# Kernel optimization log

Measured on AMD Instinct MI355X. Metric: run time of the kernel, lower is better.

Reference implementation:

```python
import jax, jax.numpy as jnp
import numpy as np

S_LEN = 256   # seq_len
B = 512       # batch
STATE = 32    # state_dim
ZD = 64       # z_dim
RNN = 512     # rnn_dim
HD = 512      # h_dim
LOG2PI = float(np.log(2.0 * np.pi))


def setup_inputs() -> dict:
    key = jax.random.key(0)
    ks = jax.random.split(key, 12)

    def mat(k, shape, fan_in):
        return jax.random.normal(k, shape, dtype=jnp.float32) * (1.0 / np.sqrt(fan_in))

    z32 = lambda *s: jnp.zeros(s, jnp.float32)
    return {
        "states": jax.random.normal(ks[0], (S_LEN, B, STATE), jnp.float32),
        "z": jax.random.normal(ks[1], (B, ZD), jnp.float32),
        # GRU layer 0: input = concat(state, action) -> 2*STATE
        "Wih0": mat(ks[2], (3 * RNN, 2 * STATE), 2 * STATE),
        "Whh0": mat(ks[3], (3 * RNN, RNN), RNN),
        "bih0": z32(3 * RNN),
        "bhh0": z32(3 * RNN),
        # GRU layer 1: input = hidden of layer 0
        "Wih1": mat(ks[4], (3 * RNN, RNN), RNN),
        "Whh1": mat(ks[5], (3 * RNN, RNN), RNN),
        "bih1": z32(3 * RNN),
        "bhh1": z32(3 * RNN),
        # dec_action_fc: Linear(STATE+ZD+RNN -> HD), ReLU, Linear(HD -> HD), ReLU
        "Wfc1": mat(ks[6], (HD, STATE + ZD + RNN), STATE + ZD + RNN),
        "bfc1": z32(HD),
        "Wfc2": mat(ks[7], (HD, HD), HD),
        "bfc2": z32(HD),
        "Wmean": mat(ks[8], (STATE, HD), HD),
        "bmean": z32(STATE),
        "Wlv": mat(ks[9], (STATE, HD), HD),
        "blv": z32(STATE),
    }


def _gru_step(x, h, Wih, Whh, bih, bhh):
    # PyTorch GRUCell math
    gi = x @ Wih.T + bih  # [B, 3R]
    gh = h @ Whh.T + bhh
    ir, iz, inn = jnp.split(gi, 3, axis=1)
    hr, hz, hn = jnp.split(gh, 3, axis=1)
    r = jax.nn.sigmoid(ir + hr)
    zg = jax.nn.sigmoid(iz + hz)
    n = jnp.tanh(inn + r * hn)
    return (1.0 - zg) * n + zg * h


def reference(states, z, Wih0, Whh0, bih0, bhh0, Wih1, Whh1, bih1, bhh1,
              Wfc1, bfc1, Wfc2, bfc2, Wmean, bmean, Wlv, blv):
    # actions[t] = states[t+1] - states[t]
    actions = states[1:] - states[:-1]
    # loop runs for actions.size(0)-1 = T-2 steps using (states[t], actions[t])
    xs = (states[:-2], actions[:-1])
    Bb = z.shape[0]
    R = Whh0.shape[1]
    h_init = jnp.zeros((2, Bb, R), states.dtype)
    nll_init = jnp.zeros((Bb, states.shape[-1]), states.dtype)

    def step(carry, xt):
        h, nll = carry
        s, a = xt  # [B, STATE] each
        # decode_action: cat(state, z, hidden[-1]) -> MLP -> mean, logvar
        fc_in = jnp.concatenate([s, z, h[1]], axis=1)
        dh = jax.nn.relu(fc_in @ Wfc1.T + bfc1)
        dh = jax.nn.relu(dh @ Wfc2.T + bfc2)
        mean = dh @ Wmean.T + bmean
        logvar = dh @ Wlv.T + blv
        # nll -= Normal(mean, logvar).log_prob(action), std = exp(0.5*logvar)
        nll_t = 0.5 * ((a - mean) ** 2 * jnp.exp(-logvar) + logvar + LOG2PI)
        # update_hidden_state with cat(state, action) through 2-layer GRU
        x_in = jnp.concatenate([s, a], axis=1)
        h0n = _gru_step(x_in, h[0], Wih0, Whh0, bih0, bhh0)
        h1n = _gru_step(h0n, h[1], Wih1, Whh1, bih1, bhh1)
        return (jnp.stack([h0n, h1n]), nll + nll_t), None

    (h, nll), _ = jax.lax.scan(step, (h_init, nll_init), xs)
    return nll  # accumulated NLL, shape [B, STATE]
```

## Files before the change

kernel.cpp:

```cpp
#include <hip/hip_runtime.h>
#include <math.h>

#define BATCH 512
#define LOG2PI 1.8378770664093453f

typedef __attribute__((ext_vector_type(8))) short bfrag;
typedef __attribute__((ext_vector_type(4))) float f32x4;
typedef __attribute__((ext_vector_type(4))) unsigned int u32x4;

#define MFMA(a,b,c) __builtin_amdgcn_mfma_f32_16x16x32_bf16(a,b,c,0,0,0)
#define ASTORE(p,v) __hip_atomic_store((p),(v),__ATOMIC_RELAXED,__HIP_MEMORY_SCOPE_AGENT)
#define ALOAD(p)    __hip_atomic_load((p),__ATOMIC_RELAXED,__HIP_MEMORY_SCOPE_AGENT)

__device__ __forceinline__ void st16_sc1(void* p, u32x4 v){
  asm volatile("global_store_dwordx4 %0, %1, off sc1" :: "v"(p), "v"(v) : "memory");
}

__device__ __forceinline__ float sigm(float x){ return 1.0f/(1.0f+__expf(-x)); }
__device__ __forceinline__ unsigned short f2bf(float f){
  unsigned int u = __builtin_bit_cast(unsigned int, f);
  u += 0x7FFFu + ((u>>16)&1u);
  return (unsigned short)(u>>16);
}
__device__ __forceinline__ bfrag cvt8(const float* __restrict__ p){
  bfrag v;
  #pragma unroll
  for (int e=0;e<8;++e) v[e] = (short)f2bf(p[e]);
  return v;
}
__device__ __forceinline__ bfrag cvt8d(const float* __restrict__ p1, const float* __restrict__ p0){
  bfrag v;
  #pragma unroll
  for (int e=0;e<8;++e) v[e] = (short)f2bf(p1[e]-p0[e]);
  return v;
}

__device__ __forceinline__ void gsync(unsigned* flags, unsigned* phase, unsigned tgt) {
  __syncthreads();
  const int tid = threadIdx.x;
  if (blockIdx.x == 0) {
    if (tid < 64) {
      if (tid == 0) ASTORE(&flags[0], tgt);
      unsigned spin = 0;
      while (true) {
        bool ok = true;
        #pragma unroll
        for (int g = 0; g < 4; ++g)
          ok &= (ALOAD(&flags[(g*64 + tid)*16]) >= tgt);
        if (__all(ok)) break;
        if (++spin > (1u<<26)) break;
        __builtin_amdgcn_s_sleep(1);
      }
      if (tid == 0) ASTORE(phase, tgt);
    }
  } else if (tid == 0) {
    ASTORE(&flags[blockIdx.x*16], tgt);
    unsigned spin = 0;
    while (ALOAD(phase) < tgt) {
      if (++spin > (1u<<26)) break;
      __builtin_amdgcn_s_sleep(1);
    }
  }
  __syncthreads();
  if (tid < 64) __builtin_amdgcn_fence(__ATOMIC_ACQUIRE, "agent");
  __syncthreads();
}

struct Params {
  const float *states, *zin;
  const float *Wih0, *Whh0, *bih0, *bhh0;
  const float *Wih1, *Whh1, *bih1, *bhh1;
  const float *Wfc1, *bfc1, *Wfc2, *bfc2;
  const float *Wmean, *bmean, *Wlv, *blv;
  unsigned short *h0b0, *h0b1, *h1b0, *h1b1;
  unsigned short *dh1b0, *dh1b1, *dh2b0, *dh2b1;
  float *out;
};

__global__ __launch_bounds__(256, 1) void fused(Params P, unsigned* flags, unsigned* phase) {
  __shared__ unsigned short sm[74752];
  const int tid  = threadIdx.x;
  const int lane = tid & 63;
  const int wv   = tid >> 6;
  const int r16  = lane & 15, kg = lane >> 4;
  const int blk  = blockIdx.x;
  const int xg   = blk & 7, sub = blk >> 3;

  unsigned short* h0b[2]  = {P.h0b0, P.h0b1};
  unsigned short* h1b[2]  = {P.h1b0, P.h1b1};
  unsigned short* dh1b[2] = {P.dh1b0, P.dh1b1};
  unsigned short* dh2b[2] = {P.dh2b0, P.dh2b1};

  if (xg < 4) {
    const int jt = sub;
    const float* Wsrc[2] = {P.Wih1, P.Whh1};
    #pragma unroll
    for (int m = 0; m < 2; ++m) {
      const float* W = Wsrc[m];
      for (int c = tid; c < 3072; c += 256) {
        int g = c >> 10, rem = c & 1023;
        int r = rem >> 6, k = (rem & 63) << 3;
        *(bfrag*)&sm[(g*16+r)*1032 + m*512 + k] =
          cvt8(&W[((size_t)(g*512 + jt*16 + r))*512 + k]);
      }
    }
  } else if (xg < 6) {
    const int jt = sub;
    for (int c = tid; c < 384; c += 256) {
      int g = c >> 7, rem = c & 127;
      int r = rem >> 3, k = (rem & 7) << 3;
      *(bfrag*)&sm[(g*16+r)*584 + k] =
        cvt8(&P.Wih0[((size_t)(g*512 + jt*16 + r))*64 + k]);
    }
    for (int c = tid; c < 3072; c += 256) {
      int g = c >> 10, rem = c & 1023;
      int r = rem >> 6, k = (rem & 63) << 3;
      *(bfrag*)&sm[(g*16+r)*584 + 64 + k] =
        cvt8(&P.Whh0[((size_t)(g*512 + jt*16 + r))*512 + k]);
    }
  } else if (xg == 6) {
    const int bn = (sub & 7) * 64;
    const int bmB = (sub >> 3) * 128;
    for (int c = tid; c < 4864; c += 256) {
      int n = c / 76, k = (c % 76) << 3;
      *(bfrag*)&sm[n*616 + k] = cvt8(&P.Wfc1[(size_t)(bn + n)*608 + k]);
    }
    for (int c = tid; c < 1024; c += 256) {
      int r = c >> 3, k = (c & 7) << 3;
      *(bfrag*)&sm[47616 + r*64 + k] = cvt8(&P.zin[(size_t)(bmB + r)*64 + k]);
    }
  } else {
    const int bn = (sub & 7) * 64;
    for (int c = tid; c < 4096; c += 256) {
      int n = c >> 6, k = (c & 63) << 3;
      *(bfrag*)&sm[n*520 + k] = cvt8(&P.Wfc2[(size_t)(bn + n)*512 + k]);
    }
    for (int c = tid; c < 4096; c += 256) {
      int m = c >> 6, k = (c & 63) << 3;
      const float* src = (m < 32) ? &P.Wmean[(size_t)m*512 + k]
                                  : &P.Wlv[(size_t)(m-32)*512 + k];
      *(bfrag*)&sm[33280 + m*520 + k] = cvt8(src);
    }
  }

  float b0 = 0.f, b1 = 0.f, b2 = 0.f, b3 = 0.f;
  if (xg < 4) {
    int j = sub*16 + r16;
    b0 = P.bih1[j] + P.bhh1[j];
    b1 = P.bih1[j+512] + P.bhh1[j+512];
    b2 = P.bih1[j+1024]; b3 = P.bhh1[j+1024];
  } else if (xg < 6) {
    int j = sub*16 + r16;
    b0 = P.bih0[j] + P.bhh0[j];
    b1 = P.bih0[j+512] + P.bhh0[j+512];
    b2 = P.bih0[j+1024]; b3 = P.bhh0[j+1024];
  } else if (xg == 6) {
    int nn0 = (sub & 7)*64 + (wv&1)*32 + r16;
    b0 = P.bfc1[nn0]; b1 = P.bfc1[nn0+16];
  } else {
    int nn0 = (sub & 7)*64 + (wv&1)*32 + r16;
    b0 = P.bfc2[nn0]; b1 = P.bfc2[nn0+16];
    int c = wv*16 + r16;
    b2 = (c < 32) ? P.bmean[c] : P.blv[c-32];
  }
  float hs[4][4] = {};
  float nacc0 = 0.f, nacc1 = 0.f;

  for (int u = 0; u <= 256; ++u) {
    gsync(flags, phase, (unsigned)(u+1));
    if (xg < 4) {
      if (u >= 1 && u <= 254) {
        const int jt = sub, bmB = xg * 128;
        const unsigned short* h0r = h0b[(u-1)&1];
        const unsigned short* h1r = h1b[u&1];
        f32x4 R[2]={}, Z[2]={}, NI[2]={}, NH[2]={};
        const int row0 = bmB + wv*32 + r16;
        #pragma unroll
        for (int half = 0; half < 2; ++half) {
          const unsigned short* asrc = half ? h1r : h0r;
          #pragma unroll 4
          for (int kt = 0; kt < 16; ++kt) {
            const int kk = kt*32 + kg*8;
            const int kl = half*512 + kk;
            bfrag a0 = *(const bfrag*)&asrc[(size_t)row0*512 + kk];
            bfrag a1 = *(const bfrag*)&asrc[(size_t)(row0+16)*512 + kk];
            bfrag bR = *(const bfrag*)&sm[(0*16+r16)*1032 + kl];
            bfrag bZ = *(const bfrag*)&sm[(1*16+r16)*1032 + kl];
            bfrag bN = *(const bfrag*)&sm[(2*16+r16)*1032 + kl];
            R[0]=MFMA(a0,bR,R[0]); R[1]=MFMA(a1,bR,R[1]);
            Z[0]=MFMA(a0,bZ,Z[0]); Z[1]=MFMA(a1,bZ,Z[1]);
            if (!half) { NI[0]=MFMA(a0,bN,NI[0]); NI[1]=MFMA(a1,bN,NI[1]); }
            else       { NH[0]=MFMA(a0,bN,NH[0]); NH[1]=MFMA(a1,bN,NH[1]); }
          }
        }
        unsigned short* exch = sm + 49536;
        #pragma unroll
        for (int fm = 0; fm < 2; ++fm)
          #pragma unroll
          for (int e = 0; e < 4; ++e) {
            int rl = wv*32 + fm*16 + kg*4 + e;
            float r  = sigm(R[fm][e] + b0);
            float zg = sigm(Z[fm][e] + b1);
            float nn = tanhf(NI[fm][e] + b2 + r*(NH[fm][e] + b3));
            float hn = (1.f - zg)*nn + zg*hs[fm][e];
            hs[fm][e] = hn;
            exch[rl*16 + r16] = f2bf(hn);
          }
        __syncthreads();
        {
          unsigned short* dst = h1b[(u-1)&1];
          int r = tid >> 1, hc = tid & 1;
          u32x4 v = *(const u32x4*)&exch[r*16 + hc*8];
          st16_sc1(dst + ((size_t)(bmB + r))*512 + jt*16 + hc*8, v);
        }
      }
    } else if (xg < 6) {
      if (u <= 253) {
        const int jt = sub, bmB = (xg - 4) * 256;
        const unsigned short* h0r = h0b[(u-1)&1];
        const float* s0 = P.states + (size_t)u*BATCH*32;
        f32x4 R[4]={}, Z[4]={}, NI[4]={}, NH[4]={};
        #pragma unroll
        for (int ks = 0; ks < 2; ++ks) {
          const int kl = ks*32 + kg*8;
          bfrag a[4];
          #pragma unroll
          for (int fm = 0; fm < 4; ++fm) {
            int row = bmB + wv*64 + fm*16 + r16;
            a[fm] = (ks == 0)
              ? cvt8(&s0[(size_t)row*32 + kg*8])
              : cvt8d(&s0[(size_t)(BATCH + row)*32 + kg*8], &s0[(size_t)row*32 + kg*8]);
          }
          bfrag bR = *(const bfrag*)&sm[(0*16+r16)*584 + kl];
          bfrag bZ = *(const bfrag*)&sm[(1*16+r16)*584 + kl];
          bfrag bN = *(const bfrag*)&sm[(2*16+r16)*584 + kl];
          #pragma unroll
          for (int fm = 0; fm < 4; ++fm) {
            R[fm]=MFMA(a[fm],bR,R[fm]); Z[fm]=MFMA(a[fm],bZ,Z[fm]); NI[fm]=MFMA(a[fm],bN,NI[fm]);
          }
        }
        #pragma unroll 2
        for (int kt = 0; kt < 16; ++kt) {
          const int kk = kt*32 + kg*8;
          const int kl = 64 + kk;
          bfrag a[4];
          #pragma unroll
          for (int fm = 0; fm < 4; ++fm) {
            int row = bmB + wv*64 + fm*16 + r16;
            a[fm] = *(const bfrag*)&h0r[(size_t)row*512 + kk];
          }
          bfrag bR = *(const bfrag*)&sm[(0*16+r16)*584 + kl];
          bfrag bZ = *(const bfrag*)&sm[(1*16+r16)*584 + kl];
          bfrag bN = *(const bfrag*)&sm[(2*16+r16)*584 + kl];
          #pragma unroll
          for (int fm = 0; fm < 4; ++fm) {
            R[fm]=MFMA(a[fm],bR,R[fm]); Z[fm]=MFMA(a[fm],bZ,Z[fm]); NH[fm]=MFMA(a[fm],bN,NH[fm]);
          }
        }
        unsigned short* exch = sm + 28032;
        #pragma unroll
        for (int fm = 0; fm < 4; ++fm)
          #pragma unroll
          for (int e = 0; e < 4; ++e) {
            int rl = wv*64 + fm*16 + kg*4 + e;
            float r  = sigm(R[fm][e] + b0);
            float zg = sigm(Z[fm][e] + b1);
            float nn = tanhf(NI[fm][e] + b2 + r*(NH[fm][e] + b3));
            float hn = (1.f - zg)*nn + zg*hs[fm][e];
            hs[fm][e] = hn;
            exch[rl*16 + r16] = f2bf(hn);
          }
        __syncthreads();
        {
          unsigned short* dst = h0b[u&1];
          int r = tid;
          u32x4 v0 = *(const u32x4*)&exch[r*16];
          u32x4 v1 = *(const u32x4*)&exch[r*16 + 8];
          unsigned short* dp = dst + ((size_t)(bmB + r))*512 + jt*16;
          st16_sc1(dp,     v0);
          st16_sc1(dp + 8, v1);
        }
      }
    } else if (xg == 6) {
      if (u >= 1 && u <= 254) {
        const int bmB = (sub >> 3) * 128, bnB = (sub & 7) * 64;
        const unsigned short* h1r = h1b[u&1];
        const float* s0 = P.states + (size_t)(u-1)*BATCH*32;
        f32x4 acc[4][2] = {};
        const int arow = bmB + (wv>>1)*64;
        const int bcol = (wv&1)*32;
        #pragma unroll 2
        for (int kt = 0; kt < 19; ++kt) {
          const int k = kt*32 + kg*8;
          bfrag a[4];
          #pragma unroll
          for (int fm = 0; fm < 4; ++fm) {
            int row = arow + fm*16 + r16;
            int rl  = row - bmB;
            if (kt == 0)      a[fm] = cvt8(&s0[(size_t)row*32 + k]);
            else if (kt <= 2) a[fm] = *(const bfrag*)&sm[47616 + rl*64 + (k - 32)];
            else              a[fm] = *(const bfrag*)&h1r[(size_t)row*512 + (k - 96)];
          }
          bfrag bf0 = *(const bfrag*)&sm[(bcol      + r16)*616 + k];
          bfrag bf1 = *(const bfrag*)&sm[(bcol + 16 + r16)*616 + k];
          #pragma unroll
          for (int fm = 0; fm < 4; ++fm) {
            acc[fm][0] = MFMA(a[fm], bf0, acc[fm][0]);
            acc[fm][1] = MFMA(a[fm], bf1, acc[fm][1]);
          }
        }
        unsigned short* exch = sm + 39424;
        #pragma unroll
        for (int fm = 0; fm < 4; ++fm)
          #pragma unroll
          for (int fn = 0; fn < 2; ++fn) {
            float bias = fn ? b1 : b0;
            #pragma unroll
            for (int e = 0; e < 4; ++e) {
              int rl = (wv>>1)*64 + fm*16 + kg*4 + e;
              int cl = bcol + fn*16 + r16;
              exch[rl*64 + cl] = f2bf(fmaxf(acc[fm][fn][e] + bias, 0.f));
            }
          }
        __syncthreads();
        {
          unsigned short* dst = dh1b[(u-1)&1];
          int r = tid >> 1, hc = tid & 1;
          #pragma unroll
          for (int q = 0; q < 4; ++q) {
            u32x4 v = *(const u32x4*)&exch[r*64 + hc*32 + q*8];
            st16_sc1(dst + ((size_t)(bmB + r))*512 + bnB + hc*32 + q*8, v);
          }
        }
        __syncthreads();
      }
    } else {
      if (u >= 2 && u <= 255) {
        const int bmB = (sub >> 3) * 128, bnB = (sub & 7) * 64;
        const unsigned short* dr = dh1b[u&1];
        f32x4 acc[4][2] = {};
        const int arow = bmB + (wv>>1)*64;
        const int bcol = (wv&1)*32;
        #pragma unroll 2
        for (int kt = 0; kt < 16; ++kt) {
          const int k = kt*32 + kg*8;
          bfrag a[4];
          #pragma unroll
          for (int fm = 0; fm < 4; ++fm) {
            int row = arow + fm*16 + r16;
            a[fm] = *(const bfrag*)&dr[(size_t)row*512 + k];
          }
          bfrag bf0 = *(const bfrag*)&sm[(bcol      + r16)*520 + k];
          bfrag bf1 = *(const bfrag*)&sm[(bcol + 16 + r16)*520 + k];
          #pragma unroll
          for (int fm = 0; fm < 4; ++fm) {
            acc[fm][0] = MFMA(a[fm], bf0, acc[fm][0]);
            acc[fm][1] = MFMA(a[fm], bf1, acc[fm][1]);
          }
        }
        unsigned short* exch = sm + 66560;
        #pragma unroll
        for (int fm = 0; fm < 4; ++fm)
          #pragma unroll
          for (int fn = 0; fn < 2; ++fn) {
            float bias = fn ? b1 : b0;
            #pragma unroll
            for (int e = 0; e < 4; ++e) {
              int rl = (wv>>1)*64 + fm*16 + kg*4 + e;
              int cl = bcol + fn*16 + r16;
              exch[rl*64 + cl] = f2bf(fmaxf(acc[fm][fn][e] + bias, 0.f));
            }
          }
        __syncthreads();
        {
          unsigned short* dst = dh2b[u&1];
          int r = tid >> 1, hc = tid & 1;
          #pragma unroll
          for (int q = 0; q < 4; ++q) {
            u32x4 v = *(const u32x4*)&exch[r*64 + hc*32 + q*8];
            st16_sc1(dst + ((size_t)(bmB + r))*512 + bnB + hc*32 + q*8, v);
          }
        }
      }
      if (u >= 3) {
        const int t = u - 3;
        const unsigned short* dr = dh2b[(u-1)&1];
        f32x4 acc = {};
        #pragma unroll 2
        for (int kt = 0; kt < 16; ++kt) {
          const int k = kt*32 + kg*8;
          bfrag a = *(const bfrag*)&dr[(size_t)(sub*16 + r16)*512 + k];
          bfrag b = *(const bfrag*)&sm[33280 + (wv*16 + r16)*520 + k];
          acc = MFMA(a, b, acc);
        }
        __syncthreads();
        float* exch = (float*)(sm + 66560);
        const int c = wv*16 + r16;
        #pragma unroll
        for (int e = 0; e < 4; ++e)
          exch[(kg*4+e)*66 + c] = acc[e] + b2;
        __syncthreads();
        const float* s0 = P.states + (size_t)t*BATCH*32;
        #pragma unroll
        for (int e2 = 0; e2 < 2; ++e2) {
          int idx = tid*2 + e2;
          int r = idx >> 5, i = idx & 31;
          int b = sub*16 + r;
          float mean = exch[r*66 + i], lv = exch[r*66 + 32 + i];
          float av = s0[(size_t)(BATCH + b)*32 + i] - s0[(size_t)b*32 + i];
          float d = av - mean;
          float v = 0.5f*(d*d*__expf(-lv) + lv + LOG2PI);
          if (e2) nacc1 += v; else nacc0 += v;
        }
      }
    }
  }

  if (xg == 7) {
    #pragma unroll
    for (int e2 = 0; e2 < 2; ++e2) {
      int idx = tid*2 + e2;
      int b = sub*16 + (idx >> 5), i = idx & 31;
      P.out[(size_t)b*32 + i] = e2 ? nacc1 : nacc0;
    }
  }
}

extern "C" void kernel_launch(void* const* d_in, const int* in_sizes, int n_in,
                              void* d_out, int out_size, void* d_ws, size_t ws_size,
                              hipStream_t stream) {
  Params P;
  P.states = (const float*)d_in[0];
  P.zin    = (const float*)d_in[1];
  P.Wih0   = (const float*)d_in[2];
  P.Whh0   = (const float*)d_in[3];
  P.bih0   = (const float*)d_in[4];
  P.bhh0   = (const float*)d_in[5];
  P.Wih1   = (const float*)d_in[6];
  P.Whh1   = (const float*)d_in[7];
  P.bih1   = (const float*)d_in[8];
  P.bhh1   = (const float*)d_in[9];
  P.Wfc1   = (const float*)d_in[10];
  P.bfc1   = (const float*)d_in[11];
  P.Wfc2   = (const float*)d_in[12];
  P.bfc2   = (const float*)d_in[13];
  P.Wmean  = (const float*)d_in[14];
  P.bmean  = (const float*)d_in[15];
  P.Wlv    = (const float*)d_in[16];
  P.blv    = (const float*)d_in[17];
  P.out = (float*)d_out;

  const size_t HB = (size_t)512*512;
  unsigned short* u = (unsigned short*)d_ws;
  P.h0b0 = u;        P.h0b1 = u + HB;
  P.h1b0 = u + 2*HB; P.h1b1 = u + 3*HB;
  P.dh1b0 = u + 4*HB; P.dh1b1 = u + 5*HB;
  P.dh2b0 = u + 6*HB; P.dh2b1 = u + 7*HB;
  unsigned* flags = (unsigned*)(u + 8*HB);
  unsigned* phase = flags + 256*16;

  hipMemsetAsync(u, 0, 4*HB*sizeof(unsigned short), stream);
  hipMemsetAsync(flags, 0, (256*16 + 16)*sizeof(unsigned), stream);
  hipMemsetAsync(d_out, 0, (size_t)out_size*sizeof(float), stream);

  fused<<<dim3(256), dim3(256), 0, stream>>>(P, flags, phase);
}
```

Baseline: 4.660 ms.

## Replace global barrier with per-producer dataflow flags and triple-buffered activations

Removes the centralized grid barrier, where block 0 polled every block and then released them all. Each block now waits only on the specific producer blocks whose outputs it reads, checking their flags at step u or u-1, and publishes its own flag after finishing the step. Activation buffers go from double to triple buffering so that blocks up to one step apart do not overwrite data still being read. This cuts the barrier's round-trip latency and lets stages drift relative to each other, at the cost of more workspace and intricate dependency indexing that must be exactly right for correctness.

```diff
diff --git a/kernel.cpp b/kernel.cpp
--- a/kernel.cpp
+++ b/kernel.cpp
@@ -33,37 +33,6 @@
   #pragma unroll
   for (int e=0;e<8;++e) v[e] = (short)f2bf(p1[e]-p0[e]);
   return v;
-}
-
-__device__ __forceinline__ void gsync(unsigned* flags, unsigned* phase, unsigned tgt) {
-  __syncthreads();
-  const int tid = threadIdx.x;
-  if (blockIdx.x == 0) {
-    if (tid < 64) {
-      if (tid == 0) ASTORE(&flags[0], tgt);
-      unsigned spin = 0;
-      while (true) {
-        bool ok = true;
-        #pragma unroll
-        for (int g = 0; g < 4; ++g)
-          ok &= (ALOAD(&flags[(g*64 + tid)*16]) >= tgt);
-        if (__all(ok)) break;
-        if (++spin > (1u<<26)) break;
-        __builtin_amdgcn_s_sleep(1);
-      }
-      if (tid == 0) ASTORE(phase, tgt);
-    }
-  } else if (tid == 0) {
-    ASTORE(&flags[blockIdx.x*16], tgt);
-    unsigned spin = 0;
-    while (ALOAD(phase) < tgt) {
-      if (++spin > (1u<<26)) break;
-      __builtin_amdgcn_s_sleep(1);
-    }
-  }
-  __syncthreads();
-  if (tid < 64) __builtin_amdgcn_fence(__ATOMIC_ACQUIRE, "agent");
-  __syncthreads();
 }
 
 struct Params {
@@ -72,12 +41,14 @@
   const float *Wih1, *Whh1, *bih1, *bhh1;
   const float *Wfc1, *bfc1, *Wfc2, *bfc2;
   const float *Wmean, *bmean, *Wlv, *blv;
-  unsigned short *h0b0, *h0b1, *h1b0, *h1b1;
-  unsigned short *dh1b0, *dh1b1, *dh2b0, *dh2b1;
+  unsigned short *h0x0, *h0x1, *h0x2;
+  unsigned short *h1x0, *h1x1, *h1x2;
+  unsigned short *d1x0, *d1x1, *d1x2;
+  unsigned short *d2x0, *d2x1, *d2x2;
   float *out;
 };
 
-__global__ __launch_bounds__(256, 1) void fused(Params P, unsigned* flags, unsigned* phase) {
+__global__ __launch_bounds__(256, 1) void fused(Params P, unsigned* flags) {
   __shared__ unsigned short sm[74752];
   const int tid  = threadIdx.x;
   const int lane = tid & 63;
@@ -86,10 +57,10 @@
   const int blk  = blockIdx.x;
   const int xg   = blk & 7, sub = blk >> 3;
 
-  unsigned short* h0b[2]  = {P.h0b0, P.h0b1};
-  unsigned short* h1b[2]  = {P.h1b0, P.h1b1};
-  unsigned short* dh1b[2] = {P.dh1b0, P.dh1b1};
-  unsigned short* dh2b[2] = {P.dh2b0, P.dh2b1};
+  unsigned short* h0b[3]  = {P.h0x0, P.h0x1, P.h0x2};
+  unsigned short* h1b[3]  = {P.h1x0, P.h1x1, P.h1x2};
+  unsigned short* dh1b[3] = {P.d1x0, P.d1x1, P.d1x2};
+  unsigned short* dh2b[3] = {P.d2x0, P.d2x1, P.d2x2};
 
   if (xg < 4) {
     const int jt = sub;
@@ -167,12 +138,44 @@
   float nacc0 = 0.f, nacc1 = 0.f;
 
   for (int u = 0; u <= 256; ++u) {
-    gsync(flags, phase, (unsigned)(u+1));
+    if (wv == 0) {
+      int pb1 = -1, pb2 = -1;
+      const unsigned t1 = (unsigned)u, t2 = (unsigned)(u - 1);
+      if (xg >= 4 && xg < 6) {
+        if (u >= 1 && lane < 32) pb1 = lane*8 + xg;
+        if (u >= 2)              pb2 = (lane>>1)*8 + 2*(xg-4) + (lane&1);
+      } else if (xg < 4) {
+        if (u >= 1) pb1 = (lane < 32) ? lane*8 + xg : (lane-32)*8 + 4 + (xg>>1);
+        if (u >= 2 && lane < 8) pb2 = (xg*8 + lane)*8 + 6;
+      } else if (xg == 6) {
+        if (u >= 1 && lane < 32) pb1 = lane*8 + (sub>>3);
+        if (u >= 2 && lane < 8)  pb2 = ((sub & ~7) + lane)*8 + 7;
+      } else {
+        if (u >= 1 && lane < 16) pb1 = ((sub & ~7) + (lane&7))*8 + ((lane<8)?6:7);
+      }
+      unsigned spin = 0;
+      while (true) {
+        bool ok = true;
+        if (pb1 >= 0) ok &= (ALOAD(&flags[pb1*16]) >= t1);
+        if (pb2 >= 0) ok &= (ALOAD(&flags[pb2*16]) >= t2);
+        if (__all(ok)) break;
+        if (++spin > (1u<<26)) break;
+        __builtin_amdgcn_s_sleep(1);
+      }
+    }
+    __syncthreads();
+    if (tid < 64) __builtin_amdgcn_fence(__ATOMIC_ACQUIRE, "agent");
+    __syncthreads();
+
+    const int iu   = u % 3;
+    const int ium1 = (u+2) % 3;
+    const int ium2 = (u+1) % 3;
+
     if (xg < 4) {
       if (u >= 1 && u <= 254) {
         const int jt = sub, bmB = xg * 128;
-        const unsigned short* h0r = h0b[(u-1)&1];
-        const unsigned short* h1r = h1b[u&1];
+        const unsigned short* h0r = h0b[ium1];
+        const unsigned short* h1r = h1b[ium2];
         f32x4 R[2]={}, Z[2]={}, NI[2]={}, NH[2]={};
         const int row0 = bmB + wv*32 + r16;
         #pragma unroll
@@ -208,7 +211,7 @@
           }
         __syncthreads();
         {
-          unsigned short* dst = h1b[(u-1)&1];
+          unsigned short* dst = h1b[ium1];
           int r = tid >> 1, hc = tid & 1;
           u32x4 v = *(const u32x4*)&exch[r*16 + hc*8];
           st16_sc1(dst + ((size_t)(bmB + r))*512 + jt*16 + hc*8, v);
@@ -217,7 +220,7 @@
     } else if (xg < 6) {
       if (u <= 253) {
         const int jt = sub, bmB = (xg - 4) * 256;
-        const unsigned short* h0r = h0b[(u-1)&1];
+        const unsigned short* h0r = h0b[ium1];
         const float* s0 = P.states + (size_t)u*BATCH*32;
         f32x4 R[4]={}, Z[4]={}, NI[4]={}, NH[4]={};
         #pragma unroll
@@ -272,7 +275,7 @@
           }
         __syncthreads();
         {
-          unsigned short* dst = h0b[u&1];
+          unsigned short* dst = h0b[iu];
           int r = tid;
           u32x4 v0 = *(const u32x4*)&exch[r*16];
           u32x4 v1 = *(const u32x4*)&exch[r*16 + 8];
@@ -284,7 +287,7 @@
     } else if (xg == 6) {
       if (u >= 1 && u <= 254) {
         const int bmB = (sub >> 3) * 128, bnB = (sub & 7) * 64;
-        const unsigned short* h1r = h1b[u&1];
+        const unsigned short* h1r = h1b[ium2];
         const float* s0 = P.states + (size_t)(u-1)*BATCH*32;
         f32x4 acc[4][2] = {};
         const int arow = bmB + (wv>>1)*64;
@@ -324,7 +327,7 @@
           }
         __syncthreads();
         {
-          unsigned short* dst = dh1b[(u-1)&1];
+          unsigned short* dst = dh1b[ium1];
           int r = tid >> 1, hc = tid & 1;
           #pragma unroll
           for (int q = 0; q < 4; ++q) {
@@ -337,7 +340,7 @@
     } else {
       if (u >= 2 && u <= 255) {
         const int bmB = (sub >> 3) * 128, bnB = (sub & 7) * 64;
-        const unsigned short* dr = dh1b[u&1];
+        const unsigned short* dr = dh1b[ium2];
         f32x4 acc[4][2] = {};
         const int arow = bmB + (wv>>1)*64;
         const int bcol = (wv&1)*32;
@@ -373,7 +376,7 @@
           }
         __syncthreads();
         {
-          unsigned short* dst = dh2b[u&1];
+          unsigned short* dst = dh2b[ium2];
           int r = tid >> 1, hc = tid & 1;
           #pragma unroll
           for (int q = 0; q < 4; ++q) {
@@ -384,7 +387,7 @@
       }
       if (u >= 3) {
         const int t = u - 3;
-        const unsigned short* dr = dh2b[(u-1)&1];
+        const unsigned short* dr = dh2b[iu];
         f32x4 acc = {};
         #pragma unroll 2
         for (int kt = 0; kt < 16; ++kt) {
@@ -414,6 +417,9 @@
         }
       }
     }
+
+    __syncthreads();
+    if (tid == 0) ASTORE(&flags[blk*16], (unsigned)(u+1));
   }
 
   if (xg == 7) {
@@ -452,16 +458,15 @@
 
   const size_t HB = (size_t)512*512;
   unsigned short* u = (unsigned short*)d_ws;
-  P.h0b0 = u;        P.h0b1 = u + HB;
-  P.h1b0 = u + 2*HB; P.h1b1 = u + 3*HB;
-  P.dh1b0 = u + 4*HB; P.dh1b1 = u + 5*HB;
-  P.dh2b0 = u + 6*HB; P.dh2b1 = u + 7*HB;
-  unsigned* flags = (unsigned*)(u + 8*HB);
-  unsigned* phase = flags + 256*16;
-
-  hipMemsetAsync(u, 0, 4*HB*sizeof(unsigned short), stream);
-  hipMemsetAsync(flags, 0, (256*16 + 16)*sizeof(unsigned), stream);
+  P.h0x0 = u;        P.h0x1 = u + HB;   P.h0x2 = u + 2*HB;
+  P.h1x0 = u + 3*HB; P.h1x1 = u + 4*HB; P.h1x2 = u + 5*HB;
+  P.d1x0 = u + 6*HB; P.d1x1 = u + 7*HB; P.d1x2 = u + 8*HB;
+  P.d2x0 = u + 9*HB; P.d2x1 = u + 10*HB; P.d2x2 = u + 11*HB;
+  unsigned* flags = (unsigned*)(u + 12*HB);
+
+  hipMemsetAsync(u, 0, 6*HB*sizeof(unsigned short), stream);
+  hipMemsetAsync(flags, 0, 256*16*sizeof(unsigned), stream);
   hipMemsetAsync(d_out, 0, (size_t)out_size*sizeof(float), stream);
 
-  fused<<<dim3(256), dim3(256), 0, stream>>>(P, flags, phase);
-}
+  fused<<<dim3(256), dim3(256), 0, stream>>>(P, flags);
+}
```

After: 4.368 ms. -6.3%, faster.
